# Kernel tuning notes

Hardware: AMD Instinct MI355X
Metric: run time of the kernel (lower is better)

The kernel has to match this reference:

```python
import jax, jax.numpy as jnp
import numpy as np

N_NODES, N_EDGES, IN_DIM, HID, N_FEAT_CLOSE, N_GRAPHS = 100000, 1600000, 128, 64, 5, 512


def _glorot(k, shape):
    lim = float(np.sqrt(6.0 / (shape[0] + shape[1])))
    return jax.random.uniform(k, shape, jnp.float32, -lim, lim)


def setup_inputs() -> dict:
    key = jax.random.key(0)
    ks = jax.random.split(key, 16)
    x = jax.random.normal(ks[0], (N_NODES, IN_DIM), jnp.float32)
    edge_index = jax.random.randint(ks[1], (2, N_EDGES), 0, N_NODES, jnp.int32)
    closeness = jax.random.uniform(ks[2], (N_NODES, N_FEAT_CLOSE), jnp.float32)
    batch = jnp.sort(jax.random.randint(ks[3], (N_NODES,), 0, N_GRAPHS, jnp.int32))
    return {
        'x': x, 'edge_index': edge_index, 'closeness': closeness, 'batch': batch,
        'num_graphs': N_GRAPHS,
        'W1': _glorot(ks[4], (IN_DIM, HID)), 'b1': jnp.zeros((HID,), jnp.float32),
        'W2': _glorot(ks[5], (HID, HID)), 'b2': jnp.zeros((HID,), jnp.float32),
        'W3': _glorot(ks[6], (HID, HID)), 'b3': jnp.zeros((HID,), jnp.float32),
        'Wc': _glorot(ks[7], (N_FEAT_CLOSE, 1)), 'bc': jnp.zeros((1,), jnp.float32),
        'Wa1': _glorot(ks[8], (HID, 16)), 'ba1': jnp.zeros((16,), jnp.float32),
        'Wa2': _glorot(ks[9], (16, 1)), 'ba2': jnp.zeros((1,), jnp.float32),
    }


def reference(x, edge_index, closeness, batch, num_graphs, W1, b1, W2, b2, W3, b3, Wc, bc, Wa1, ba1, Wa2, ba2):
    src, dst = edge_index[0], edge_index[1]
    N = x.shape[0]
    # GCN symmetric normalization with implicit self-loops (weight 1)
    deg = jax.ops.segment_sum(jnp.ones(src.shape, x.dtype), dst, num_segments=N) + 1.0
    dinv = jax.lax.rsqrt(deg)
    norm = dinv[src] * dinv[dst]  # [E]
    self_norm = (dinv * dinv)[:, None]  # 1/deg, self-loop coefficient

    def gcn(h, W, b):
        h = h @ W  # [N, hid]
        agg = jax.ops.segment_sum(h[src] * norm[:, None], dst, num_segments=N)
        return jax.nn.relu(agg + h * self_norm + b)

    h = gcn(x, W1, b1)
    h = gcn(h, W2, b2)
    h = gcn(h, W3, b3)

    # per-graph softmax over closeness scores, scaled by graph size
    s = closeness @ Wc + bc  # [N,1]
    smax = jax.ops.segment_max(s, batch, num_segments=num_graphs)
    e = jnp.exp(s - smax[batch])
    ssum = jax.ops.segment_sum(e, batch, num_segments=num_graphs)
    counts = jax.ops.segment_sum(jnp.ones((N,), x.dtype), batch, num_segments=num_graphs)
    w = (e / ssum[batch]) * counts[batch][:, None]  # [N,1]

    # weighted per-graph max pooling, then tiny MLP per graph
    pooled = jax.ops.segment_max(w * h, batch, num_segments=num_graphs)  # [G,64]
    a = jax.nn.relu(pooled @ Wa1 + ba1)
    return a @ Wa2 + ba2  # [G,1]
```

## Files before the change

kernel.cpp:

```cpp
#include <hip/hip_runtime.h>

#define N_NODESC 100000
#define N_EDGESC 1600000
#define IN_DIMC 128
#define HIDC 64
#define N_GRAPHSC 512
#define PAD_DEG 64

__device__ __forceinline__ unsigned enc_f32(float f) {
  unsigned b = __float_as_uint(f);
  return (b & 0x80000000u) ? ~b : (b | 0x80000000u);
}
__device__ __forceinline__ float dec_f32(unsigned k) {
  unsigned b = (k & 0x80000000u) ? (k & 0x7fffffffu) : ~k;
  return __uint_as_float(b);
}


__global__ void zero_kernel(int* cnt, unsigned* smax, float* ssum, int* cntg, unsigned* pooled) {
  int i = blockIdx.x * blockDim.x + threadIdx.x;
  if (i < N_NODESC) cnt[i] = 0;
  if (i < N_GRAPHSC) { smax[i] = 0u; ssum[i] = 0.f; cntg[i] = 0; }
  if (i < N_GRAPHSC * HIDC) pooled[i] = 0u;
}

__global__ void build_kernel(const int* __restrict__ srcv, const int* __restrict__ dstv,
                             int* __restrict__ cnt, int* __restrict__ csr_pad) {
  int e = blockIdx.x * blockDim.x + threadIdx.x;
  if (e >= N_EDGESC) return;
  int d = dstv[e];
  int s = atomicAdd(&cnt[d], 1);
  if (s < PAD_DEG)
    __builtin_nontemporal_store(srcv[e], &csr_pad[d * PAD_DEG + s]);
}

__global__ void dinv_kernel(const int* __restrict__ cnt, float* __restrict__ dinv) {
  int i = blockIdx.x * blockDim.x + threadIdx.x;
  if (i < N_NODESC) dinv[i] = rsqrtf((float)cnt[i] + 1.0f);
}


#define GT_M 128
#define XS_LD 132
template <int KT>
__global__ void __launch_bounds__(256, 3)
gemm_tile_kernel(const float* __restrict__ X, const float* __restrict__ W,
                 const float* __restrict__ dinv, float* __restrict__ T) {
  __shared__ float xs[64 * XS_LD];
  __shared__ float ws[64 * 64];
  int t = threadIdx.x;
  int base = blockIdx.x * GT_M;
  int r0 = (t >> 4) * 8;
  int c0 = (t & 15) * 4;
  float acc[8][4];
#pragma unroll
  for (int i = 0; i < 8; ++i)
#pragma unroll
    for (int j = 0; j < 4; ++j) acc[i][j] = 0.f;

  int kq = (t & 15) * 4;
  int rr = t >> 4;

  for (int kb = 0; kb < KT; kb += 64) {
    if (kb) __syncthreads();
#pragma unroll
    for (int it = 0; it < 8; ++it) {
      int r = rr + it * 16;
      int grow = base + r;
      if (grow >= N_NODESC) grow = N_NODESC - 1;
      float4 q = *(const float4*)(X + (size_t)grow * KT + kb + kq);
      xs[(kq + 0) * XS_LD + r] = q.x;
      xs[(kq + 1) * XS_LD + r] = q.y;
      xs[(kq + 2) * XS_LD + r] = q.z;
      xs[(kq + 3) * XS_LD + r] = q.w;
    }
#pragma unroll
    for (int it = 0; it < 4; ++it) {
      int idx = (it * 256 + t) * 4;
      *(float4*)(ws + idx) = *(const float4*)(W + (size_t)kb * HIDC + idx);
    }
    __syncthreads();
#pragma unroll 8
    for (int k = 0; k < 64; ++k) {
      float4 xa = *(const float4*)(xs + k * XS_LD + r0);
      float4 xb = *(const float4*)(xs + k * XS_LD + r0 + 4);
      float4 wf = *(const float4*)(ws + k * 64 + c0);
      float xf[8] = {xa.x, xa.y, xa.z, xa.w, xb.x, xb.y, xb.z, xb.w};
      float wv[4] = {wf.x, wf.y, wf.z, wf.w};
#pragma unroll
      for (int i = 0; i < 8; ++i)
#pragma unroll
        for (int j = 0; j < 4; ++j) acc[i][j] = fmaf(xf[i], wv[j], acc[i][j]);
    }
  }
#pragma unroll
  for (int i = 0; i < 8; ++i) {
    int row = base + r0 + i;
    if (row < N_NODESC) {
      float dv = dinv[row];
      float4 o;
      o.x = acc[i][0] * dv;
      o.y = acc[i][1] * dv;
      o.z = acc[i][2] * dv;
      o.w = acc[i][3] * dv;
      *(float4*)(T + (size_t)row * HIDC + c0) = o;
    }
  }
}

__global__ void gather_kernel(const float* __restrict__ ts, const float* __restrict__ dinv,
                              const int* __restrict__ cnt, const int* __restrict__ csr_pad,
                              const float* __restrict__ bias, float* __restrict__ h) {
  int lane = threadIdx.x & 63;
  int node = (blockIdx.x * blockDim.x + threadIdx.x) >> 6;
  if (node >= N_NODESC) return;
  int deg = min(cnt[node], PAD_DEG);
  const int* __restrict__ row = csr_pad + node * PAD_DEG;
  float sum = ts[node * HIDC + lane];
  int e = 0;
  for (; e + 8 <= deg; e += 8) {
    int s0 = row[e], s1 = row[e + 1], s2 = row[e + 2], s3 = row[e + 3];
    int s4 = row[e + 4], s5 = row[e + 5], s6 = row[e + 6], s7 = row[e + 7];
    float v0 = ts[s0 * HIDC + lane];
    float v1 = ts[s1 * HIDC + lane];
    float v2 = ts[s2 * HIDC + lane];
    float v3 = ts[s3 * HIDC + lane];
    float v4 = ts[s4 * HIDC + lane];
    float v5 = ts[s5 * HIDC + lane];
    float v6 = ts[s6 * HIDC + lane];
    float v7 = ts[s7 * HIDC + lane];
    sum += ((v0 + v1) + (v2 + v3)) + ((v4 + v5) + (v6 + v7));
  }
  for (; e + 4 <= deg; e += 4) {
    int s0 = row[e], s1 = row[e + 1], s2 = row[e + 2], s3 = row[e + 3];
    float v0 = ts[s0 * HIDC + lane];
    float v1 = ts[s1 * HIDC + lane];
    float v2 = ts[s2 * HIDC + lane];
    float v3 = ts[s3 * HIDC + lane];
    sum += (v0 + v1) + (v2 + v3);
  }
  for (; e < deg; ++e) sum += ts[row[e] * HIDC + lane];
  h[node * HIDC + lane] = fmaxf(sum * dinv[node] + bias[lane], 0.f);
}


__global__ void score_kernel(const float* __restrict__ closeness, const float* __restrict__ Wc,
                             const float* __restrict__ bc, const int* __restrict__ batch,
                             float* __restrict__ sbuf, unsigned* __restrict__ smax,
                             int* __restrict__ cntg) {
  int i = blockIdx.x * blockDim.x + threadIdx.x;
  int lane = threadIdx.x & 63;
  bool valid = i < N_NODESC;
  float s = 0.f;
  int g = 0;
  unsigned key = 0u;
  if (valid) {
    s = bc[0];
#pragma unroll
    for (int k = 0; k < 5; ++k) s += closeness[i * 5 + k] * Wc[k];
    sbuf[i] = s;
    g = batch[i];
    key = enc_f32(s);
  }
  bool fullwave = ((i - lane) + 64) <= N_NODESC;
  int g0 = __shfl(g, 0);
  int g63 = __shfl(g, 63);
  if (fullwave && g0 == g63) {
    unsigned kmax = key;
#pragma unroll
    for (int off = 32; off > 0; off >>= 1) kmax = max(kmax, (unsigned)__shfl_xor((int)kmax, off));
    if (lane == 0) {
      atomicMax(&smax[g], kmax);
      atomicAdd(&cntg[g], 64);
    }
  } else if (valid) {
    atomicMax(&smax[g], key);
    atomicAdd(&cntg[g], 1);
  }
}

__global__ void expsum_kernel(const float* __restrict__ sbuf, const unsigned* __restrict__ smax,
                              const int* __restrict__ batch, float* __restrict__ ebuf,
                              float* __restrict__ ssum) {
  int i = blockIdx.x * blockDim.x + threadIdx.x;
  int lane = threadIdx.x & 63;
  bool valid = i < N_NODESC;
  float ev = 0.f;
  int g = 0;
  if (valid) {
    g = batch[i];
    float m = dec_f32(smax[g]);
    ev = expf(sbuf[i] - m);
    ebuf[i] = ev;
  }
  bool fullwave = ((i - lane) + 64) <= N_NODESC;
  int g0 = __shfl(g, 0);
  int g63 = __shfl(g, 63);
  if (fullwave && g0 == g63) {
    float tot = ev;
#pragma unroll
    for (int off = 32; off > 0; off >>= 1) tot += __shfl_xor(tot, off);
    if (lane == 0) unsafeAtomicAdd(&ssum[g], tot);
  } else if (valid) {
    unsafeAtomicAdd(&ssum[g], ev);
  }
}

#define POOL_CHUNK 32
__global__ void pool_kernel(const float* __restrict__ h, const float* __restrict__ ebuf,
                            const float* __restrict__ ssum, const int* __restrict__ cntg,
                            const int* __restrict__ batch, unsigned* __restrict__ pooled) {
  int lane = threadIdx.x & 63;
  int wave = (blockIdx.x * blockDim.x + threadIdx.x) >> 6;
  int nw = (gridDim.x * blockDim.x) >> 6;
  for (int base = wave * POOL_CHUNK; base < N_NODESC; base += nw * POOL_CHUNK) {
    int end = min(base + POOL_CHUNK, N_NODESC);
    int curg = batch[base];
    float vmax = 0.f;
    for (int i = base; i < end; ++i) {
      int g = batch[i];
      if (g != curg) {
        atomicMax(&pooled[curg * HIDC + lane], __float_as_uint(vmax));
        vmax = 0.f;
        curg = g;
      }
      float w = ebuf[i] / ssum[g] * (float)cntg[g];
      vmax = fmaxf(vmax, w * h[i * HIDC + lane]);
    }
    atomicMax(&pooled[curg * HIDC + lane], __float_as_uint(vmax));
  }
}

__global__ void mlp_kernel(const unsigned* __restrict__ pooled, const float* __restrict__ Wa1,
                           const float* __restrict__ ba1, const float* __restrict__ Wa2,
                           const float* __restrict__ ba2, float* __restrict__ out) {
  int lane = threadIdx.x & 63;
  int g = (blockIdx.x * blockDim.x + threadIdx.x) >> 6;
  if (g >= N_GRAPHSC) return;
  float p = __uint_as_float(pooled[g * HIDC + lane]);
  float o = 0.f;
#pragma unroll
  for (int t = 0; t < 16; ++t) {
    float prod = p * Wa1[lane * 16 + t];
#pragma unroll
    for (int off = 32; off > 0; off >>= 1) prod += __shfl_xor(prod, off);
    float a = fmaxf(prod + ba1[t], 0.f);
    o += a * Wa2[t];
  }
  if (lane == 0) out[g] = o + ba2[0];
}


extern "C" void kernel_launch(void* const* d_in, const int* in_sizes, int n_in,
                              void* d_out, int out_size, void* d_ws, size_t ws_size,
                              hipStream_t stream) {
  const float* x = (const float*)d_in[0];
  const int* ei = (const int*)d_in[1];
  const float* closeness = (const float*)d_in[2];
  const int* batch = (const int*)d_in[3];
  const float* W1 = (const float*)d_in[5];
  const float* b1 = (const float*)d_in[6];
  const float* W2 = (const float*)d_in[7];
  const float* b2 = (const float*)d_in[8];
  const float* W3 = (const float*)d_in[9];
  const float* b3 = (const float*)d_in[10];
  const float* Wc = (const float*)d_in[11];
  const float* bc = (const float*)d_in[12];
  const float* Wa1 = (const float*)d_in[13];
  const float* ba1 = (const float*)d_in[14];
  const float* Wa2 = (const float*)d_in[15];
  const float* ba2 = (const float*)d_in[16];
  float* out = (float*)d_out;
  const int* srcv = ei;
  const int* dstv = ei + N_EDGESC;

  char* ws = (char*)d_ws;
  size_t off = 0;
  auto alloc = [&](size_t bytes) -> void* {
    void* p = ws + off;
    off = (off + bytes + 255) & ~(size_t)255;
    return p;
  };
  float* tbuf = (float*)alloc(sizeof(float) * N_NODESC * HIDC);
  float* hbuf = (float*)alloc(sizeof(float) * N_NODESC * HIDC);
  int* csr_pad = (int*)alloc(sizeof(int) * N_NODESC * PAD_DEG);
  int* cnt = (int*)alloc(sizeof(int) * N_NODESC);
  float* dinv = (float*)alloc(sizeof(float) * N_NODESC);
  float* sbuf = (float*)alloc(sizeof(float) * N_NODESC);
  float* ebuf = (float*)alloc(sizeof(float) * N_NODESC);
  unsigned* smax = (unsigned*)alloc(sizeof(unsigned) * N_GRAPHSC);
  float* ssum = (float*)alloc(sizeof(float) * N_GRAPHSC);
  int* cntg = (int*)alloc(sizeof(int) * N_GRAPHSC);
  unsigned* pooled = (unsigned*)alloc(sizeof(unsigned) * N_GRAPHSC * HIDC);

  const int B = 256;
  int gN = (N_NODESC + B - 1) / B;
  int gE = (N_EDGESC + B - 1) / B;
  int gGather = (N_NODESC * 64) / B;
  int gTile = (N_NODESC + GT_M - 1) / GT_M;

  zero_kernel<<<gN, B, 0, stream>>>(cnt, smax, ssum, cntg, pooled);
  build_kernel<<<gE, B, 0, stream>>>(srcv, dstv, cnt, csr_pad);
  dinv_kernel<<<gN, B, 0, stream>>>(cnt, dinv);

  gemm_tile_kernel<IN_DIMC><<<gTile, B, 0, stream>>>(x, W1, dinv, tbuf);
  gather_kernel<<<gGather, B, 0, stream>>>(tbuf, dinv, cnt, csr_pad, b1, hbuf);
  gemm_tile_kernel<HIDC><<<gTile, B, 0, stream>>>(hbuf, W2, dinv, tbuf);
  gather_kernel<<<gGather, B, 0, stream>>>(tbuf, dinv, cnt, csr_pad, b2, hbuf);
  gemm_tile_kernel<HIDC><<<gTile, B, 0, stream>>>(hbuf, W3, dinv, tbuf);
  gather_kernel<<<gGather, B, 0, stream>>>(tbuf, dinv, cnt, csr_pad, b3, hbuf);

  score_kernel<<<gN, B, 0, stream>>>(closeness, Wc, bc, batch, sbuf, smax, cntg);
  expsum_kernel<<<gN, B, 0, stream>>>(sbuf, smax, batch, ebuf, ssum);
  pool_kernel<<<782, B, 0, stream>>>(hbuf, ebuf, ssum, cntg, batch, pooled);
  mlp_kernel<<<(N_GRAPHSC * 64) / B, B, 0, stream>>>(pooled, Wa1, ba1, Wa2, ba2, out);
}
```

Measured before the change: 596.8 us.

## Fuse graph readout into one per-graph block kernel and split CSR build

Measured after the change: 525.1 us. 1.14x faster.

```diff
diff --git a/kernel.cpp b/kernel.cpp
--- a/kernel.cpp
+++ b/kernel.cpp
@@ -7,36 +7,44 @@
 #define N_GRAPHSC 512
 #define PAD_DEG 64
 
-__device__ __forceinline__ unsigned enc_f32(float f) {
-  unsigned b = __float_as_uint(f);
-  return (b & 0x80000000u) ? ~b : (b | 0x80000000u);
-}
-__device__ __forceinline__ float dec_f32(unsigned k) {
-  unsigned b = (k & 0x80000000u) ? (k & 0x7fffffffu) : ~k;
-  return __uint_as_float(b);
-}
-
-
-__global__ void zero_kernel(int* cnt, unsigned* smax, float* ssum, int* cntg, unsigned* pooled) {
+
+__global__ void zero_kernel(int* cnt) {
   int i = blockIdx.x * blockDim.x + threadIdx.x;
   if (i < N_NODESC) cnt[i] = 0;
-  if (i < N_GRAPHSC) { smax[i] = 0u; ssum[i] = 0.f; cntg[i] = 0; }
-  if (i < N_GRAPHSC * HIDC) pooled[i] = 0u;
-}
-
-__global__ void build_kernel(const int* __restrict__ srcv, const int* __restrict__ dstv,
-                             int* __restrict__ cnt, int* __restrict__ csr_pad) {
+}
+
+__global__ void deg_kernel(const int* __restrict__ dstv, int* __restrict__ cnt,
+                           int* __restrict__ slot) {
   int e = blockIdx.x * blockDim.x + threadIdx.x;
-  if (e >= N_EDGESC) return;
-  int d = dstv[e];
-  int s = atomicAdd(&cnt[d], 1);
-  if (s < PAD_DEG)
-    __builtin_nontemporal_store(srcv[e], &csr_pad[d * PAD_DEG + s]);
+  if (e < N_EDGESC) slot[e] = atomicAdd(&cnt[dstv[e]], 1);
+}
+
+__global__ void fill_pad_kernel(const int* __restrict__ srcv, const int* __restrict__ dstv,
+                                const int* __restrict__ slot, int* __restrict__ csr_pad) {
+  int e4 = (blockIdx.x * blockDim.x + threadIdx.x) * 4;
+  if (e4 >= N_EDGESC) return;
+  int4 s = *(const int4*)(srcv + e4);
+  int4 d = *(const int4*)(dstv + e4);
+  int4 sl = *(const int4*)(slot + e4);
+  if (sl.x < PAD_DEG) __builtin_nontemporal_store(s.x, &csr_pad[d.x * PAD_DEG + sl.x]);
+  if (sl.y < PAD_DEG) __builtin_nontemporal_store(s.y, &csr_pad[d.y * PAD_DEG + sl.y]);
+  if (sl.z < PAD_DEG) __builtin_nontemporal_store(s.z, &csr_pad[d.z * PAD_DEG + sl.z]);
+  if (sl.w < PAD_DEG) __builtin_nontemporal_store(s.w, &csr_pad[d.w * PAD_DEG + sl.w]);
 }
 
 __global__ void dinv_kernel(const int* __restrict__ cnt, float* __restrict__ dinv) {
   int i = blockIdx.x * blockDim.x + threadIdx.x;
   if (i < N_NODESC) dinv[i] = rsqrtf((float)cnt[i] + 1.0f);
+}
+
+__global__ void bounds_kernel(const int* __restrict__ batch, int* __restrict__ gstart) {
+  int i = blockIdx.x * blockDim.x + threadIdx.x;
+  if (i >= N_NODESC) return;
+  int b = batch[i];
+  int prev = (i == 0) ? -1 : batch[i - 1];
+  for (int g = prev + 1; g <= b; ++g) gstart[g] = i;
+  if (i == N_NODESC - 1)
+    for (int g = b + 1; g <= N_GRAPHSC; ++g) gstart[g] = N_NODESC;
 }
 
 
@@ -143,111 +151,72 @@
   h[node * HIDC + lane] = fmaxf(sum * dinv[node] + bias[lane], 0.f);
 }
 
-
-__global__ void score_kernel(const float* __restrict__ closeness, const float* __restrict__ Wc,
-                             const float* __restrict__ bc, const int* __restrict__ batch,
-                             float* __restrict__ sbuf, unsigned* __restrict__ smax,
-                             int* __restrict__ cntg) {
-  int i = blockIdx.x * blockDim.x + threadIdx.x;
-  int lane = threadIdx.x & 63;
-  bool valid = i < N_NODESC;
-  float s = 0.f;
-  int g = 0;
-  unsigned key = 0u;
-  if (valid) {
-    s = bc[0];
-#pragma unroll
-    for (int k = 0; k < 5; ++k) s += closeness[i * 5 + k] * Wc[k];
-    sbuf[i] = s;
-    g = batch[i];
-    key = enc_f32(s);
-  }
-  bool fullwave = ((i - lane) + 64) <= N_NODESC;
-  int g0 = __shfl(g, 0);
-  int g63 = __shfl(g, 63);
-  if (fullwave && g0 == g63) {
-    unsigned kmax = key;
-#pragma unroll
-    for (int off = 32; off > 0; off >>= 1) kmax = max(kmax, (unsigned)__shfl_xor((int)kmax, off));
-    if (lane == 0) {
-      atomicMax(&smax[g], kmax);
-      atomicAdd(&cntg[g], 64);
-    }
-  } else if (valid) {
-    atomicMax(&smax[g], key);
-    atomicAdd(&cntg[g], 1);
-  }
-}
-
-__global__ void expsum_kernel(const float* __restrict__ sbuf, const unsigned* __restrict__ smax,
-                              const int* __restrict__ batch, float* __restrict__ ebuf,
-                              float* __restrict__ ssum) {
-  int i = blockIdx.x * blockDim.x + threadIdx.x;
-  int lane = threadIdx.x & 63;
-  bool valid = i < N_NODESC;
-  float ev = 0.f;
-  int g = 0;
-  if (valid) {
-    g = batch[i];
-    float m = dec_f32(smax[g]);
-    ev = expf(sbuf[i] - m);
-    ebuf[i] = ev;
-  }
-  bool fullwave = ((i - lane) + 64) <= N_NODESC;
-  int g0 = __shfl(g, 0);
-  int g63 = __shfl(g, 63);
-  if (fullwave && g0 == g63) {
-    float tot = ev;
-#pragma unroll
-    for (int off = 32; off > 0; off >>= 1) tot += __shfl_xor(tot, off);
-    if (lane == 0) unsafeAtomicAdd(&ssum[g], tot);
-  } else if (valid) {
-    unsafeAtomicAdd(&ssum[g], ev);
-  }
-}
-
-#define POOL_CHUNK 32
-__global__ void pool_kernel(const float* __restrict__ h, const float* __restrict__ ebuf,
-                            const float* __restrict__ ssum, const int* __restrict__ cntg,
-                            const int* __restrict__ batch, unsigned* __restrict__ pooled) {
-  int lane = threadIdx.x & 63;
-  int wave = (blockIdx.x * blockDim.x + threadIdx.x) >> 6;
-  int nw = (gridDim.x * blockDim.x) >> 6;
-  for (int base = wave * POOL_CHUNK; base < N_NODESC; base += nw * POOL_CHUNK) {
-    int end = min(base + POOL_CHUNK, N_NODESC);
-    int curg = batch[base];
-    float vmax = 0.f;
-    for (int i = base; i < end; ++i) {
-      int g = batch[i];
-      if (g != curg) {
-        atomicMax(&pooled[curg * HIDC + lane], __float_as_uint(vmax));
-        vmax = 0.f;
-        curg = g;
-      }
-      float w = ebuf[i] / ssum[g] * (float)cntg[g];
-      vmax = fmaxf(vmax, w * h[i * HIDC + lane]);
-    }
-    atomicMax(&pooled[curg * HIDC + lane], __float_as_uint(vmax));
-  }
-}
-
-__global__ void mlp_kernel(const unsigned* __restrict__ pooled, const float* __restrict__ Wa1,
-                           const float* __restrict__ ba1, const float* __restrict__ Wa2,
-                           const float* __restrict__ ba2, float* __restrict__ out) {
-  int lane = threadIdx.x & 63;
-  int g = (blockIdx.x * blockDim.x + threadIdx.x) >> 6;
-  if (g >= N_GRAPHSC) return;
-  float p = __uint_as_float(pooled[g * HIDC + lane]);
-  float o = 0.f;
-#pragma unroll
-  for (int t = 0; t < 16; ++t) {
-    float prod = p * Wa1[lane * 16 + t];
-#pragma unroll
-    for (int off = 32; off > 0; off >>= 1) prod += __shfl_xor(prod, off);
-    float a = fmaxf(prod + ba1[t], 0.f);
-    o += a * Wa2[t];
-  }
-  if (lane == 0) out[g] = o + ba2[0];
+__global__ void __launch_bounds__(256)
+readout_kernel(const float* __restrict__ h, const float* __restrict__ closeness,
+               const float* __restrict__ Wc, const float* __restrict__ bc,
+               const int* __restrict__ gstart, const float* __restrict__ Wa1,
+               const float* __restrict__ ba1, const float* __restrict__ Wa2,
+               const float* __restrict__ ba2, float* __restrict__ out) {
+  __shared__ float sArr[1024];
+  __shared__ float red[256];
+  __shared__ float cross[4 * 64];
+  int g = blockIdx.x;
+  int t = threadIdx.x;
+  int n0 = gstart[g], n1 = gstart[g + 1];
+  int count = n1 - n0;
+  int cap = min(count, 1024);
+  float wc0 = Wc[0], wc1 = Wc[1], wc2 = Wc[2], wc3 = Wc[3], wc4 = Wc[4], bcv = bc[0];
+  float lmax = -3.4e38f;
+  for (int idx = t; idx < cap; idx += 256) {
+    const float* c = closeness + (size_t)(n0 + idx) * 5;
+    float s = fmaf(c[4], wc4, fmaf(c[3], wc3, fmaf(c[2], wc2, fmaf(c[1], wc1, fmaf(c[0], wc0, bcv)))));
+    sArr[idx] = s;
+    lmax = fmaxf(lmax, s);
+  }
+  red[t] = lmax;
+  __syncthreads();
+  for (int s = 128; s > 0; s >>= 1) {
+    if (t < s) red[t] = fmaxf(red[t], red[t + s]);
+    __syncthreads();
+  }
+  float m = red[0];
+  __syncthreads();
+  float lsum = 0.f;
+  for (int idx = t; idx < cap; idx += 256) {
+    float e = expf(sArr[idx] - m);
+    sArr[idx] = e;
+    lsum += e;
+  }
+  red[t] = lsum;
+  __syncthreads();
+  for (int s = 128; s > 0; s >>= 1) {
+    if (t < s) red[t] += red[t + s];
+    __syncthreads();
+  }
+  float scale = (count > 0) ? ((float)count / red[0]) : 0.f;
+  __syncthreads();
+  int wv = t >> 6, lane = t & 63;
+  float pmax = 0.f;
+  for (int idx = wv; idx < cap; idx += 4) {
+    float w = sArr[idx] * scale;
+    pmax = fmaxf(pmax, w * h[(size_t)(n0 + idx) * HIDC + lane]);
+  }
+  cross[wv * 64 + lane] = pmax;
+  __syncthreads();
+  if (wv == 0) {
+    float p = fmaxf(fmaxf(cross[lane], cross[64 + lane]),
+                    fmaxf(cross[128 + lane], cross[192 + lane]));
+    float o = 0.f;
+#pragma unroll
+    for (int tt = 0; tt < 16; ++tt) {
+      float prod = p * Wa1[lane * 16 + tt];
+#pragma unroll
+      for (int off = 32; off > 0; off >>= 1) prod += __shfl_xor(prod, off);
+      float a = fmaxf(prod + ba1[tt], 0.f);
+      o += a * Wa2[tt];
+    }
+    if (lane == 0) out[g] = o + ba2[0];
+  }
 }
 
 
@@ -284,24 +253,23 @@
   float* tbuf = (float*)alloc(sizeof(float) * N_NODESC * HIDC);
   float* hbuf = (float*)alloc(sizeof(float) * N_NODESC * HIDC);
   int* csr_pad = (int*)alloc(sizeof(int) * N_NODESC * PAD_DEG);
+  int* slot = (int*)alloc(sizeof(int) * N_EDGESC);
   int* cnt = (int*)alloc(sizeof(int) * N_NODESC);
   float* dinv = (float*)alloc(sizeof(float) * N_NODESC);
-  float* sbuf = (float*)alloc(sizeof(float) * N_NODESC);
-  float* ebuf = (float*)alloc(sizeof(float) * N_NODESC);
-  unsigned* smax = (unsigned*)alloc(sizeof(unsigned) * N_GRAPHSC);
-  float* ssum = (float*)alloc(sizeof(float) * N_GRAPHSC);
-  int* cntg = (int*)alloc(sizeof(int) * N_GRAPHSC);
-  unsigned* pooled = (unsigned*)alloc(sizeof(unsigned) * N_GRAPHSC * HIDC);
+  int* gstart = (int*)alloc(sizeof(int) * (N_GRAPHSC + 1));
 
   const int B = 256;
   int gN = (N_NODESC + B - 1) / B;
   int gE = (N_EDGESC + B - 1) / B;
+  int gE4 = (N_EDGESC / 4 + B - 1) / B;
   int gGather = (N_NODESC * 64) / B;
   int gTile = (N_NODESC + GT_M - 1) / GT_M;
 
-  zero_kernel<<<gN, B, 0, stream>>>(cnt, smax, ssum, cntg, pooled);
-  build_kernel<<<gE, B, 0, stream>>>(srcv, dstv, cnt, csr_pad);
+  zero_kernel<<<gN, B, 0, stream>>>(cnt);
+  deg_kernel<<<gE, B, 0, stream>>>(dstv, cnt, slot);
+  fill_pad_kernel<<<gE4, B, 0, stream>>>(srcv, dstv, slot, csr_pad);
   dinv_kernel<<<gN, B, 0, stream>>>(cnt, dinv);
+  bounds_kernel<<<gN, B, 0, stream>>>(batch, gstart);
 
   gemm_tile_kernel<IN_DIMC><<<gTile, B, 0, stream>>>(x, W1, dinv, tbuf);
   gather_kernel<<<gGather, B, 0, stream>>>(tbuf, dinv, cnt, csr_pad, b1, hbuf);
@@ -310,8 +278,6 @@
   gemm_tile_kernel<HIDC><<<gTile, B, 0, stream>>>(hbuf, W3, dinv, tbuf);
   gather_kernel<<<gGather, B, 0, stream>>>(tbuf, dinv, cnt, csr_pad, b3, hbuf);
 
-  score_kernel<<<gN, B, 0, stream>>>(closeness, Wc, bc, batch, sbuf, smax, cntg);
-  expsum_kernel<<<gN, B, 0, stream>>>(sbuf, smax, batch, ebuf, ssum);
-  pool_kernel<<<782, B, 0, stream>>>(hbuf, ebuf, ssum, cntg, batch, pooled);
-  mlp_kernel<<<(N_GRAPHSC * 64) / B, B, 0, stream>>>(pooled, Wa1, ba1, Wa2, ba2, out);
-}
+  readout_kernel<<<N_GRAPHSC, B, 0, stream>>>(hbuf, closeness, Wc, bc, gstart,
+                                              Wa1, ba1, Wa2, ba2, out);
+}
```
